# Optimization experiments

Hardware: AMD Instinct MI355X
Metric: run time of the kernel (lower is better)

Reference implementation:

```python
import jax, jax.numpy as jnp
import numpy as np

BLOCK = 128
SPARSE_BLOCK = 128
SF = 4
NEG = jnp.finfo(jnp.float32).min


def _unfold(x, size, step):
    # x: (..., T, d) -> (..., b, size, d) overlapping windows (torch unfold + transpose)
    b = (x.shape[-2] - size) // step + 1
    idx = np.arange(b)[:, None] * step + np.arange(size)
    return x[..., idx, :]


def _pad_tokens(x, s, pad_value):
    cfg = [(0, 0)] * (x.ndim - 2) + [(s, s), (0, 0)]
    return jnp.pad(x, cfg, constant_values=pad_value)


def _local_blocks(x, pad_value):
    size, step = BLOCK * 3, BLOCK
    s = (size - step) // 2
    return _unfold(_pad_tokens(x, s, pad_value), size, step)


def _sparse_blocks(x, pad_value):
    size0, step = SPARSE_BLOCK * 3, BLOCK // SF
    odd = step % 2
    size = size0 * 2
    s = (size - step) // 2 + odd
    xw = _unfold(_pad_tokens(x, s, pad_value), size, step)
    if odd:
        xw = xw[..., :-1, :, :]
    u = (size - BLOCK * 3 // SF) // 2 + odd
    sb = SPARSE_BLOCK
    u_ = u + odd
    return jnp.concatenate([xw[..., u - sb:u, :], xw[..., -u_:-u_ + sb, :]], axis=-2)


def _cat_gsl(x_global, x_sparse, x_local):
    # x_local: (n,h,b,t_loc,d); broadcast global over block axis
    b = x_local.shape[-3]
    g = jnp.broadcast_to(x_global[..., None, :, :],
                         x_global.shape[:-2] + (b,) + x_global.shape[-2:])
    return jnp.concatenate([g, x_sparse, x_local], axis=-2)


def _build_lsg(x, x_sparse, x_global, pad_value):
    loc = _local_blocks(x, pad_value)
    sp = _sparse_blocks(x_sparse, pad_value)
    return _cat_gsl(x_global, sp, loc)


def reference(query_layer, key_layer, value_layer, attention_mask,
              sparse_key, sparse_value, sparse_mask,
              global_key, global_value, global_mask):
    n, h, t, d = query_layer.shape
    n_blocks = t // BLOCK

    keys = _build_lsg(key_layer, sparse_key, global_key, 0.0)      # (n,h,b,K,d)
    vals = _build_lsg(value_layer, sparse_value, global_value, 0.0)

    # masks: (n,1,1,T) treated as d=1 token data after transpose
    m = jnp.swapaxes(attention_mask, -1, -2)    # (n,1,t,1)
    sm = jnp.swapaxes(sparse_mask, -1, -2)      # (n,1,t/SF,1)
    gm = jnp.swapaxes(global_mask, -1, -2)      # (n,1,g,1)
    mask = _build_lsg(m, sm, gm, NEG)           # (n,1,b,K,1)
    mask = jnp.swapaxes(mask, -1, -2)           # (n,1,b,1,K)

    q = query_layer.reshape(n, h, n_blocks, BLOCK, d)
    scores = jnp.einsum('nhbqd,nhbkd->nhbqk', q, keys) / jnp.sqrt(jnp.float32(d))
    probs = jax.nn.softmax(scores + mask, axis=-1)
    ctx = jnp.einsum('nhbqk,nhbkd->nhbqd', probs, vals)
    return ctx.reshape(n, h, t, d)


def setup_inputs() -> dict:
    key = jax.random.key(0)
    n, h, t, d = 2, 12, 4096, 64
    g = 64
    ts = t // SF
    k = jax.random.split(key, 7)
    return {
        'query_layer': jax.random.normal(k[0], (n, h, t, d), jnp.float32),
        'key_layer': jax.random.normal(k[1], (n, h, t, d), jnp.float32),
        'value_layer': jax.random.normal(k[2], (n, h, t, d), jnp.float32),
        'attention_mask': jnp.zeros((n, 1, 1, t), jnp.float32),
        'sparse_key': jax.random.normal(k[3], (n, h, ts, d), jnp.float32),
        'sparse_value': jax.random.normal(k[4], (n, h, ts, d), jnp.float32),
        'sparse_mask': jnp.zeros((n, 1, 1, ts), jnp.float32),
        'global_key': jax.random.normal(k[5], (n, h, g, d), jnp.float32),
        'global_value': jax.random.normal(k[6], (n, h, g, d), jnp.float32),
        'global_mask': jnp.zeros((n, 1, 1, g), jnp.float32),
    }
```

## Files before the change

kernel.cpp:

```cpp
#include <hip/hip_runtime.h>
#include <hip/hip_bf16.h>

typedef __attribute__((ext_vector_type(8))) short short8;
typedef __attribute__((ext_vector_type(4))) float f32x4;
typedef __attribute__((ext_vector_type(4))) unsigned u32x4;

#define LOG2E 1.44269504f
#define SCL2  0.18033688f
#define MNEG  -3.0e38f
#define MINIT -1.0e30f

__device__ __forceinline__ short f2bf(float f) {
  union { float f; unsigned u; } x; x.f = f;
  return (short)((x.u + 0x7FFFu + ((x.u >> 16) & 1u)) >> 16);
}
__device__ __forceinline__ float exp2g(float x) {
  float r; asm("v_exp_f32 %0, %1" : "=v"(r) : "v"(x)); return r;
}
__device__ __forceinline__ unsigned cvt_pk_bf16(float lo, float hi) {
  unsigned r;
  asm("v_cvt_pk_bf16_f32 %0, %1, %2" : "=v"(r) : "v"(lo), "v"(hi));
  return r;
}

__device__ __forceinline__ void conv_one(
    const float* __restrict__ src, short* __restrict__ dst,
    int Tin, int pad, int cid) {
  int Tpad = Tin + 2 * pad;
  int row = cid >> 3;
  int d0 = (cid & 7) * 8;
  int tok = row % Tpad;
  int nh = row / Tpad;
  int st = tok - pad;
  short8 o;
  if (st >= 0 && st < Tin) {
    const float4* sp = (const float4*)(src + ((size_t)nh * Tin + st) * 64 + d0);
    float4 f0 = sp[0], f1 = sp[1];
    o[0] = f2bf(f0.x); o[1] = f2bf(f0.y); o[2] = f2bf(f0.z); o[3] = f2bf(f0.w);
    o[4] = f2bf(f1.x); o[5] = f2bf(f1.y); o[6] = f2bf(f1.z); o[7] = f2bf(f1.w);
  } else {
#pragma unroll
    for (int j = 0; j < 8; ++j) o[j] = 0;
  }
  *(short8*)(dst + (size_t)row * 64 + d0) = o;
}

__device__ __forceinline__ void transv_one(
    const float* __restrict__ src, short* __restrict__ dst,
    int Tin, int pad, int tiles, int bidx, int tid, short (*lt)[72]) {
  int tile = bidx % tiles;
  int nh = bidx / tiles;
  int Tpad = Tin + 2 * pad;
  int c0 = tile * 64;
  int tok = tid >> 2;
  int dc = (tid & 3) * 16;
  int st = c0 + tok - pad;
  if (st >= 0 && st < Tin) {
    const float4* sp = (const float4*)(src + ((size_t)nh * Tin + st) * 64 + dc);
#pragma unroll
    for (int i = 0; i < 4; ++i) {
      float4 f = sp[i];
      lt[tok][dc + i * 4 + 0] = f2bf(f.x);
      lt[tok][dc + i * 4 + 1] = f2bf(f.y);
      lt[tok][dc + i * 4 + 2] = f2bf(f.z);
      lt[tok][dc + i * 4 + 3] = f2bf(f.w);
    }
  } else {
#pragma unroll
    for (int i = 0; i < 16; ++i) lt[tok][dc + i] = 0;
  }
  __syncthreads();
  int d = tid >> 2;
  int tc = (tid & 3) * 16;
  short8 o0, o1;
#pragma unroll
  for (int j = 0; j < 8; ++j) { o0[j] = lt[tc + j][d]; o1[j] = lt[tc + 8 + j][d]; }
  short* dp = dst + ((size_t)nh * 64 + d) * Tpad + c0 + tc;
  *(short8*)(dp) = o0;
  *(short8*)(dp + 8) = o1;
}

__global__ __launch_bounds__(256) void prepass_all(
    const float* __restrict__ K, const float* __restrict__ SK,
    const float* __restrict__ GK,
    const float* __restrict__ V, const float* __restrict__ SV,
    const float* __restrict__ GV,
    short* __restrict__ KL, short* __restrict__ KS, short* __restrict__ KG,
    short* __restrict__ VTL, short* __restrict__ VTS, short* __restrict__ VTG,
    const float* __restrict__ am, const float* __restrict__ sm,
    const float* __restrict__ gm,
    float* __restrict__ AM2, float* __restrict__ SM2, float* __restrict__ GM2) {
  __shared__ short lt[64][72];
  int bidx = blockIdx.x;
  int tid = threadIdx.x;
  if (bidx < 3264) { conv_one(K,  KL, 4096, 128, bidx * 256 + tid); return; }
  bidx -= 3264;
  if (bidx < 1008) { conv_one(SK, KS, 1024, 160, bidx * 256 + tid); return; }
  bidx -= 1008;
  if (bidx < 48)   { conv_one(GK, KG, 64, 0, bidx * 256 + tid); return; }
  bidx -= 48;
  if (bidx < 1632) { transv_one(V,  VTL, 4096, 128, 68, bidx, tid, lt); return; }
  bidx -= 1632;
  if (bidx < 504)  { transv_one(SV, VTS, 1024, 160, 21, bidx, tid, lt); return; }
  bidx -= 504;
  if (bidx < 24)   { transv_one(GV, VTG, 64, 0, 1, bidx, tid, lt); return; }
  bidx -= 24;
  int i = bidx * 256 + tid;
  if (i < 2 * 4352) {
    int n = i / 4352, rr = i % 4352, s = rr - 128;
    AM2[i] = (s >= 0 && s < 4096) ? am[n * 4096 + s] * LOG2E : MNEG;
  } else if (i < 2 * 4352 + 2 * 1344) {
    int j = i - 2 * 4352;
    int n = j / 1344, rr = j % 1344, s = rr - 160;
    SM2[j] = (s >= 0 && s < 1024) ? sm[n * 1024 + s] * LOG2E : MNEG;
  } else {
    int j = i - 2 * 4352 - 2 * 1344;
    GM2[j] = gm[j] * LOG2E;
  }
}

__global__ __launch_bounds__(512, 4) void lsg_attn9(
    const short* __restrict__ KL, const short* __restrict__ VTL,
    const short* __restrict__ KS, const short* __restrict__ VTS,
    const short* __restrict__ KG, const short* __restrict__ VTG,
    const float* __restrict__ AM2, const float* __restrict__ SM2,
    const float* __restrict__ GM2,
    const float* __restrict__ q_, float* __restrict__ out) {
  constexpr int TPL = 4352, TPS = 1344;
  __shared__ __align__(16) char smem[35328];

  int bid = blockIdx.x;
  bid = (bid & 7) * 96 + (bid >> 3);
  const int b = bid & 31, nh = bid >> 5, n_ = nh / 12;
  const int tid = threadIdx.x;
  const int wid = tid >> 6, lane = tid & 63;
  const int c = lane & 15, g = lane >> 4;
  const int r = tid >> 3, ch = tid & 7;
  const int skey = ((r >> 5) << 5) | (((r >> 2) & 3) << 3) |
                   (((r >> 4) & 1) << 2) | (r & 3);
  float* sclw = (float*)(smem + 32768) + wid * 16;
  const unsigned stg = ((unsigned)r << 7) + ((unsigned)(ch * 16) ^ ((unsigned)(r & 7) << 4));

  unsigned long long enc = 0; int nt = 0;
  {
    auto push = [&](int t) { enc |= (unsigned long long)t << (4 * nt); ++nt; };
    push(0);
    if (b >= 4)  push(1);
    if (b >= 2)  push(2);
    if (b <= 29) push(3);
    if (b <= 27) push(4);
    if (b >= 1)  { push(5); push(6); }
    push(7); push(8);
    if (b <= 30) { push(9); push(10); }
  }

  const float* qb = q_ + ((size_t)nh * 4096 + (size_t)b * 128 + wid * 16) * 64;
  short8 qa[2];
#pragma unroll
  for (int kc = 0; kc < 2; ++kc) {
    const float* qp = qb + (size_t)c * 64 + kc * 32 + g * 8;
    float4 f0 = *(const float4*)(qp);
    float4 f1 = *(const float4*)(qp + 4);
    short8 tq;
    tq[0] = f2bf(f0.x); tq[1] = f2bf(f0.y); tq[2] = f2bf(f0.z); tq[3] = f2bf(f0.w);
    tq[4] = f2bf(f1.x); tq[5] = f2bf(f1.y); tq[6] = f2bf(f1.z); tq[7] = f2bf(f1.w);
    qa[kc] = tq;
  }

  f32x4 acc[4];
#pragma unroll
  for (int dd = 0; dd < 4; ++dd) acc[dd] = f32x4{0.f, 0.f, 0.f, 0.f};
  float mrun = MINIT, lrun = 0.f;

  auto src_for = [&](int t, const short*& kp, const short*& vp,
                     const float*& mp, int& stride) {
    if (t == 0) {
      kp = KG + (size_t)nh * (64 * 64);
      vp = VTG + (size_t)nh * (64 * 64);
      mp = GM2 + n_ * 64;
      stride = 64;
    } else if (t <= 4) {
      int r0 = b * 32 + (t - 1) * 64 + (t >= 3 ? 96 : 0);
      kp = KS + ((size_t)nh * TPS + r0) * 64;
      vp = VTS + (size_t)nh * (64 * TPS) + r0;
      mp = SM2 + n_ * TPS + r0;
      stride = TPS;
    } else {
      int r0 = b * 128 + (t - 5) * 64;
      kp = KL + ((size_t)nh * TPL + r0) * 64;
      vp = VTL + (size_t)nh * (64 * TPL) + r0;
      mp = AM2 + n_ * TPL + r0;
      stride = TPL;
    }
  };

  short8 kr, vr;

  {
    const short* kp; const short* vp; const float* mp; int st;
    src_for(0, kp, vp, mp, st);
    kr = *(const short8*)(kp + skey * 64 + ch * 8);
    vr = *(const short8*)(vp + (size_t)r * st + ch * 8);
    *(short8*)(smem + stg) = kr;
    *(short8*)(smem + 16384 + stg) = vr;
    src_for((int)((enc >> 4) & 15ull), kp, vp, mp, st);
    kr = *(const short8*)(kp + skey * 64 + ch * 8);
    vr = *(const short8*)(vp + (size_t)r * st + ch * 8);
  }

  for (int i = 0; i < nt; ++i) {
    asm volatile("s_waitcnt lgkmcnt(0)\n\ts_barrier" ::: "memory");
    const int cur = i & 1, nxt = cur ^ 1;
    char* kbuf = smem + cur * 8192;
    char* vbuf = smem + 16384 + cur * 8192;

    f32x4 mk[4];
    {
      int tl = (int)((enc >> (4 * i)) & 15ull);
      const short* kp; const short* vp; const float* mp; int st;
      src_for(tl, kp, vp, mp, st);
#pragma unroll
      for (int kt = 0; kt < 4; ++kt)
        mk[kt] = *(const f32x4*)(mp + ((kt >> 1) << 5) + g * 8 + ((kt & 1) << 2));
    }

    short8 bk[4][2];
#pragma unroll
    for (int kt = 0; kt < 4; ++kt)
#pragma unroll
      for (int kc = 0; kc < 2; ++kc) {
        unsigned off = ((unsigned)(kt * 16 + c) << 7) +
                       ((unsigned)(kc * 64 + g * 16) ^ ((unsigned)(c & 7) << 4));
        bk[kt][kc] = *(const short8*)(kbuf + off);
      }

    if (i + 1 < nt) {
      *(short8*)(smem + nxt * 8192 + stg) = kr;
      *(short8*)(smem + 16384 + nxt * 8192 + stg) = vr;
    }
    if (i + 2 < nt) {
      int tn = (int)((enc >> (4 * (i + 2))) & 15ull);
      const short* kp; const short* vp; const float* mp; int st;
      src_for(tn, kp, vp, mp, st);
      kr = *(const short8*)(kp + skey * 64 + ch * 8);
      vr = *(const short8*)(vp + (size_t)r * st + ch * 8);
    }

    f32x4 s4[4];
    __builtin_amdgcn_s_setprio(1);
#pragma unroll
    for (int kt = 0; kt < 4; ++kt) {
      f32x4 z = f32x4{0.f, 0.f, 0.f, 0.f};
      z = __builtin_amdgcn_mfma_f32_16x16x32_bf16(bk[kt][0], qa[0], z, 0, 0, 0);
      z = __builtin_amdgcn_mfma_f32_16x16x32_bf16(bk[kt][1], qa[1], z, 0, 0, 0);
      s4[kt] = z;
    }
    __builtin_amdgcn_s_setprio(0);
#pragma unroll
    for (int kt = 0; kt < 4; ++kt)
#pragma unroll
      for (int j = 0; j < 4; ++j)
        s4[kt][j] = fmaf(s4[kt][j], SCL2, mk[kt][j]);

    float rs = 0.f;
    f32x4 p4[4];
#pragma unroll
    for (int kt = 0; kt < 4; ++kt)
#pragma unroll
      for (int j = 0; j < 4; ++j) {
        float p = exp2g(s4[kt][j] - mrun);
        p4[kt][j] = p;
        rs += p;
      }

    if (__any(rs > 4096.f)) {
      float tv = s4[0][0];
#pragma unroll
      for (int kt = 0; kt < 4; ++kt)
#pragma unroll
        for (int j = 0; j < 4; ++j) tv = fmaxf(tv, s4[kt][j]);
      tv = fmaxf(tv, __shfl_xor(tv, 16));
      tv = fmaxf(tv, __shfl_xor(tv, 32));
      float mn = fmaxf(mrun, tv);
      float sc = exp2g(mrun - mn);
      if (lane < 16) sclw[lane] = sc;
      rs = 0.f;
#pragma unroll
      for (int kt = 0; kt < 4; ++kt)
#pragma unroll
        for (int j = 0; j < 4; ++j) {
          float p = exp2g(s4[kt][j] - mn);
          p4[kt][j] = p;
          rs += p;
        }
      lrun = lrun * sc + rs;
      mrun = mn;
      f32x4 sq = *(const f32x4*)&sclw[4 * g];
#pragma unroll
      for (int dd = 0; dd < 4; ++dd)
#pragma unroll
        for (int j = 0; j < 4; ++j) acc[dd][j] *= sq[j];
    } else {
      lrun += rs;
    }

#pragma unroll
    for (int kk = 0; kk < 2; ++kk) {
      u32x4 uu;
      uu[0] = cvt_pk_bf16(p4[2 * kk][0], p4[2 * kk][1]);
      uu[1] = cvt_pk_bf16(p4[2 * kk][2], p4[2 * kk][3]);
      uu[2] = cvt_pk_bf16(p4[2 * kk + 1][0], p4[2 * kk + 1][1]);
      uu[3] = cvt_pk_bf16(p4[2 * kk + 1][2], p4[2 * kk + 1][3]);
      short8 pa = __builtin_bit_cast(short8, uu);
      __builtin_amdgcn_s_setprio(1);
#pragma unroll
      for (int dd = 0; dd < 4; ++dd) {
        unsigned voff = ((unsigned)(dd * 16 + c) << 7) +
                        ((unsigned)(kk * 64 + g * 16) ^ ((unsigned)(c & 7) << 4));
        short8 bv = *(const short8*)(vbuf + voff);
        acc[dd] = __builtin_amdgcn_mfma_f32_16x16x32_bf16(pa, bv, acc[dd], 0, 0, 0);
      }
      __builtin_amdgcn_s_setprio(0);
    }
  }

  float l = lrun;
  l += __shfl_xor(l, 16);
  l += __shfl_xor(l, 32);
  if (lane < 16) sclw[lane] = 1.f / l;
  f32x4 iv = *(const f32x4*)&sclw[4 * g];
  __syncthreads();
  float* fst = (float*)smem + wid * (16 * 68);
#pragma unroll
  for (int j = 0; j < 4; ++j)
#pragma unroll
    for (int dd = 0; dd < 4; ++dd)
      fst[(4 * g + j) * 68 + dd * 16 + c] = acc[dd][j] * iv[j];
  int rr = lane >> 2, cc = lane & 3;
  const float* fs = (float*)smem + wid * (16 * 68) + rr * 68 + cc * 16;
  float* op = out + ((size_t)nh * 4096 + (size_t)b * 128 + wid * 16 + rr) * 64 + cc * 16;
#pragma unroll
  for (int i = 0; i < 4; ++i)
    *(float4*)(op + i * 4) = *(const float4*)(fs + i * 4);
}

__global__ __launch_bounds__(256) void lsg_attn_fb(
    const float* __restrict__ q_,  const float* __restrict__ k_,
    const float* __restrict__ v_,  const float* __restrict__ amask,
    const float* __restrict__ sk,  const float* __restrict__ sv,
    const float* __restrict__ smk, const float* __restrict__ gk,
    const float* __restrict__ gv,  const float* __restrict__ gmk,
    float* __restrict__ out) {
  constexpr int T = 4096, D = 64, TS = 1024;
  constexpr float NEGF = -3.402823466e38f;
  __shared__ __align__(16) short k_lds[32][72];
  __shared__ __align__(16) short v_lds[64][40];
  __shared__ __align__(16) short p_lds[4][32][40];
  __shared__ float m_lds[32];
  const int bid = blockIdx.x;
  const int b = bid & 31, nh = bid >> 5, n_ = nh / 12;
  const int tid = threadIdx.x, wid = tid >> 6, lane = tid & 63;
  const int c = lane & 15, g = lane >> 4;
  const float* qb = q_ + ((size_t)nh * T + (size_t)b * 128) * D;
  const float* kb = k_ + (size_t)nh * T * D;
  const float* vb = v_ + (size_t)nh * T * D;
  const float* skb = sk + (size_t)nh * TS * D;
  const float* svb = sv + (size_t)nh * TS * D;
  const float* gkb = gk + (size_t)nh * 64 * D;
  const float* gvb = gv + (size_t)nh * 64 * D;
  const float* am = amask + (size_t)n_ * T;
  const float* sm = smk + (size_t)n_ * TS;
  const float* gm = gmk + (size_t)n_ * 64;
  short8 qa[2][2];
#pragma unroll
  for (int mt = 0; mt < 2; ++mt)
#pragma unroll
    for (int kc = 0; kc < 2; ++kc) {
      const float* qp = qb + (size_t)(wid * 32 + mt * 16 + c) * D + kc * 32 + g * 8;
      short8 t;
#pragma unroll
      for (int j = 0; j < 8; ++j) t[j] = f2bf(qp[j]);
      qa[mt][kc] = t;
    }
  f32x4 acc[2][4];
#pragma unroll
  for (int mt = 0; mt < 2; ++mt)
#pragma unroll
    for (int dd = 0; dd < 4; ++dd) acc[mt][dd] = f32x4{0.f, 0.f, 0.f, 0.f};
  float mrun[2][4], lrun[2][4];
#pragma unroll
  for (int mt = 0; mt < 2; ++mt)
#pragma unroll
    for (int j = 0; j < 4; ++j) { mrun[mt][j] = NEGF; lrun[mt][j] = 0.f; }
  const int key_local = tid >> 3;
  const int seg = tid & 7;
  const int d0 = seg * 8;
  for (int tile = 0; tile < 22; ++tile) {
    __syncthreads();
    {
      const int kk = tile * 32 + key_local;
      const float* ksrc; const float* vsrc; float mval; bool valid;
      if (kk < 64) {
        ksrc = gkb + kk * D; vsrc = gvb + kk * D; mval = gm[kk]; valid = true;
      } else if (kk < 320) {
        int s = b * 32 - 160 + (kk - 64) + ((kk >= 192) ? 96 : 0);
        valid = (s >= 0) && (s < TS);
        int sc2 = valid ? s : 0;
        ksrc = skb + sc2 * D; vsrc = svb + sc2 * D;
        mval = valid ? sm[sc2] : NEGF;
      } else {
        int tt = b * 128 - 128 + (kk - 320);
        valid = (tt >= 0) && (tt < T);
        int tc = valid ? tt : 0;
        ksrc = kb + tc * D; vsrc = vb + tc * D;
        mval = valid ? am[tc] : NEGF;
      }
      short8 k8; short v8[8];
      if (valid) {
#pragma unroll
        for (int j = 0; j < 8; ++j) { k8[j] = f2bf(ksrc[d0 + j]); v8[j] = f2bf(vsrc[d0 + j]); }
      } else {
#pragma unroll
        for (int j = 0; j < 8; ++j) { k8[j] = 0; v8[j] = 0; }
      }
      *(short8*)(&k_lds[key_local][d0]) = k8;
#pragma unroll
      for (int j = 0; j < 8; ++j) v_lds[d0 + j][key_local] = v8[j];
      if (seg == 0) m_lds[key_local] = mval;
    }
    __syncthreads();
    short8 bk[2][2];
#pragma unroll
    for (int kt = 0; kt < 2; ++kt)
#pragma unroll
      for (int kc = 0; kc < 2; ++kc)
        bk[kt][kc] = *(const short8*)(&k_lds[kt * 16 + c][kc * 32 + g * 8]);
    f32x4 s_[2][2];
#pragma unroll
    for (int mt = 0; mt < 2; ++mt)
#pragma unroll
      for (int kt = 0; kt < 2; ++kt) {
        f32x4 z = f32x4{0.f, 0.f, 0.f, 0.f};
        z = __builtin_amdgcn_mfma_f32_16x16x32_bf16(qa[mt][0], bk[kt][0], z, 0, 0, 0);
        z = __builtin_amdgcn_mfma_f32_16x16x32_bf16(qa[mt][1], bk[kt][1], z, 0, 0, 0);
        s_[mt][kt] = z;
      }
    const float msk0 = m_lds[c];
    const float msk1 = m_lds[16 + c];
#pragma unroll
    for (int mt = 0; mt < 2; ++mt) {
#pragma unroll
      for (int j = 0; j < 4; ++j) {
        float s0 = s_[mt][0][j] * 0.125f + msk0;
        float s1 = s_[mt][1][j] * 0.125f + msk1;
        float tv = fmaxf(s0, s1);
        tv = fmaxf(tv, __shfl_xor(tv, 1));
        tv = fmaxf(tv, __shfl_xor(tv, 2));
        tv = fmaxf(tv, __shfl_xor(tv, 4));
        tv = fmaxf(tv, __shfl_xor(tv, 8));
        float mold = mrun[mt][j];
        float mnew = fmaxf(mold, tv);
        float scale = __expf(mold - mnew);
        mrun[mt][j] = mnew;
        float p0 = __expf(s0 - mnew);
        float p1 = __expf(s1 - mnew);
        lrun[mt][j] = lrun[mt][j] * scale + p0 + p1;
#pragma unroll
        for (int dd = 0; dd < 4; ++dd) acc[mt][dd][j] *= scale;
        p_lds[wid][mt * 16 + g * 4 + j][c] = f2bf(p0);
        p_lds[wid][mt * 16 + g * 4 + j][16 + c] = f2bf(p1);
      }
    }
    __syncthreads();
#pragma unroll
    for (int mt = 0; mt < 2; ++mt) {
      short8 pa = *(const short8*)(&p_lds[wid][mt * 16 + c][g * 8]);
#pragma unroll
      for (int dd = 0; dd < 4; ++dd) {
        short8 bv = *(const short8*)(&v_lds[dd * 16 + c][g * 8]);
        acc[mt][dd] = __builtin_amdgcn_mfma_f32_16x16x32_bf16(pa, bv, acc[mt][dd], 0, 0, 0);
      }
    }
  }
  float* ob = out + ((size_t)nh * T + (size_t)b * 128 + (size_t)wid * 32) * D;
#pragma unroll
  for (int mt = 0; mt < 2; ++mt)
#pragma unroll
    for (int j = 0; j < 4; ++j) {
      float l = lrun[mt][j];
      l += __shfl_xor(l, 1);
      l += __shfl_xor(l, 2);
      l += __shfl_xor(l, 4);
      l += __shfl_xor(l, 8);
      float inv = 1.f / l;
      int row = mt * 16 + g * 4 + j;
#pragma unroll
      for (int dd = 0; dd < 4; ++dd)
        ob[(size_t)row * D + dd * 16 + c] = acc[mt][dd][j] * inv;
    }
}

extern "C" void kernel_launch(void* const* d_in, const int* in_sizes, int n_in,
                              void* d_out, int out_size, void* d_ws, size_t ws_size,
                              hipStream_t stream) {
  const float* q  = (const float*)d_in[0];
  const float* k  = (const float*)d_in[1];
  const float* v  = (const float*)d_in[2];
  const float* am = (const float*)d_in[3];
  const float* sk = (const float*)d_in[4];
  const float* sv = (const float*)d_in[5];
  const float* sm = (const float*)d_in[6];
  const float* gk = (const float*)d_in[7];
  const float* gv = (const float*)d_in[8];
  const float* gm = (const float*)d_in[9];
  float* out = (float*)d_out;

  size_t off = 0;
  char* base = (char*)d_ws;
  auto alloc = [&](size_t bytes) { void* p = base + off; off += bytes; return p; };
  short* KL  = (short*)alloc(13369344);
  short* VTL = (short*)alloc(13369344);
  short* KS  = (short*)alloc(4128768);
  short* VTS = (short*)alloc(4128768);
  short* KG  = (short*)alloc(196608);
  short* VTG = (short*)alloc(196608);
  float* AM2 = (float*)alloc(34816);
  float* SM2 = (float*)alloc(10752);
  float* GM2 = (float*)alloc(512);

  if (off <= ws_size) {
    hipLaunchKernelGGL(prepass_all, dim3(6525), dim3(256), 0, stream,
                       k, sk, gk, v, sv, gv, KL, KS, KG, VTL, VTS, VTG,
                       am, sm, gm, AM2, SM2, GM2);
    hipLaunchKernelGGL(lsg_attn9, dim3(768), dim3(512), 0, stream,
                       KL, VTL, KS, VTS, KG, VTG, AM2, SM2, GM2, q, out);
  } else {
    hipLaunchKernelGGL(lsg_attn_fb, dim3(768), dim3(256), 0, stream,
                       q, k, v, am, sk, sv, sm, gk, gv, gm, out);
  }
}
```

Baseline: 58.74 us.

## Give each wave two query tiles to reuse K/V fragments, fold scale into K

The attention kernel now runs 4 waves of 256 threads, each owning 32 query rows (two 16-row MFMA tiles), so each K and V fragment read from LDS feeds two MFMAs. The softmax scale is applied to keys during the bf16 conversion prepass, and the mask is used as the MFMA accumulator init, which drops the per-score fma. The aim is fewer LDS reads per MFMA and less VALU work. In exchange each wave holds more registers (two accumulator sets), the launch bounds drop to 3 blocks per CU, and there are fewer waves to hide latency.

```diff
diff --git a/kernel.cpp b/kernel.cpp
--- a/kernel.cpp
+++ b/kernel.cpp
@@ -36,8 +36,10 @@
   if (st >= 0 && st < Tin) {
     const float4* sp = (const float4*)(src + ((size_t)nh * Tin + st) * 64 + d0);
     float4 f0 = sp[0], f1 = sp[1];
-    o[0] = f2bf(f0.x); o[1] = f2bf(f0.y); o[2] = f2bf(f0.z); o[3] = f2bf(f0.w);
-    o[4] = f2bf(f1.x); o[5] = f2bf(f1.y); o[6] = f2bf(f1.z); o[7] = f2bf(f1.w);
+    o[0] = f2bf(f0.x * SCL2); o[1] = f2bf(f0.y * SCL2);
+    o[2] = f2bf(f0.z * SCL2); o[3] = f2bf(f0.w * SCL2);
+    o[4] = f2bf(f1.x * SCL2); o[5] = f2bf(f1.y * SCL2);
+    o[6] = f2bf(f1.z * SCL2); o[7] = f2bf(f1.w * SCL2);
   } else {
 #pragma unroll
     for (int j = 0; j < 8; ++j) o[j] = 0;
@@ -119,7 +121,7 @@
   }
 }
 
-__global__ __launch_bounds__(512, 4) void lsg_attn9(
+__global__ __launch_bounds__(256, 3) void lsg_attn10(
     const short* __restrict__ KL, const short* __restrict__ VTL,
     const short* __restrict__ KS, const short* __restrict__ VTS,
     const short* __restrict__ KG, const short* __restrict__ VTG,
@@ -135,11 +137,12 @@
   const int tid = threadIdx.x;
   const int wid = tid >> 6, lane = tid & 63;
   const int c = lane & 15, g = lane >> 4;
-  const int r = tid >> 3, ch = tid & 7;
+  const int r = tid >> 2, ch = tid & 3;
   const int skey = ((r >> 5) << 5) | (((r >> 2) & 3) << 3) |
                    (((r >> 4) & 1) << 2) | (r & 3);
-  float* sclw = (float*)(smem + 32768) + wid * 16;
-  const unsigned stg = ((unsigned)r << 7) + ((unsigned)(ch * 16) ^ ((unsigned)(r & 7) << 4));
+  float* sclw = (float*)(smem + 32768) + wid * 32;
+  const unsigned stg0 = ((unsigned)r << 7) + ((unsigned)(ch * 16) ^ ((unsigned)(r & 7) << 4));
+  const unsigned stg1 = ((unsigned)r << 7) + ((unsigned)((ch + 4) * 16) ^ ((unsigned)(r & 7) << 4));
 
   unsigned long long enc = 0; int nt = 0;
   {
@@ -154,23 +157,27 @@
     if (b <= 30) { push(9); push(10); }
   }
 
-  const float* qb = q_ + ((size_t)nh * 4096 + (size_t)b * 128 + wid * 16) * 64;
-  short8 qa[2];
-#pragma unroll
-  for (int kc = 0; kc < 2; ++kc) {
-    const float* qp = qb + (size_t)c * 64 + kc * 32 + g * 8;
-    float4 f0 = *(const float4*)(qp);
-    float4 f1 = *(const float4*)(qp + 4);
-    short8 tq;
-    tq[0] = f2bf(f0.x); tq[1] = f2bf(f0.y); tq[2] = f2bf(f0.z); tq[3] = f2bf(f0.w);
-    tq[4] = f2bf(f1.x); tq[5] = f2bf(f1.y); tq[6] = f2bf(f1.z); tq[7] = f2bf(f1.w);
-    qa[kc] = tq;
-  }
-
-  f32x4 acc[4];
-#pragma unroll
-  for (int dd = 0; dd < 4; ++dd) acc[dd] = f32x4{0.f, 0.f, 0.f, 0.f};
-  float mrun = MINIT, lrun = 0.f;
+  const float* qb = q_ + ((size_t)nh * 4096 + (size_t)b * 128 + wid * 32) * 64;
+  short8 qa[2][2];
+#pragma unroll
+  for (int mt = 0; mt < 2; ++mt)
+#pragma unroll
+    for (int kc = 0; kc < 2; ++kc) {
+      const float* qp = qb + (size_t)(mt * 16 + c) * 64 + kc * 32 + g * 8;
+      float4 f0 = *(const float4*)(qp);
+      float4 f1 = *(const float4*)(qp + 4);
+      short8 tq;
+      tq[0] = f2bf(f0.x); tq[1] = f2bf(f0.y); tq[2] = f2bf(f0.z); tq[3] = f2bf(f0.w);
+      tq[4] = f2bf(f1.x); tq[5] = f2bf(f1.y); tq[6] = f2bf(f1.z); tq[7] = f2bf(f1.w);
+      qa[mt][kc] = tq;
+    }
+
+  f32x4 acc[2][4];
+#pragma unroll
+  for (int mt = 0; mt < 2; ++mt)
+#pragma unroll
+    for (int dd = 0; dd < 4; ++dd) acc[mt][dd] = f32x4{0.f, 0.f, 0.f, 0.f};
+  float mrun[2] = {MINIT, MINIT}, lrun[2] = {0.f, 0.f};
 
   auto src_for = [&](int t, const short*& kp, const short*& vp,
                      const float*& mp, int& stride) {
@@ -194,18 +201,24 @@
     }
   };
 
-  short8 kr, vr;
+  short8 kr0, kr1, vr0, vr1;
 
   {
     const short* kp; const short* vp; const float* mp; int st;
     src_for(0, kp, vp, mp, st);
-    kr = *(const short8*)(kp + skey * 64 + ch * 8);
-    vr = *(const short8*)(vp + (size_t)r * st + ch * 8);
-    *(short8*)(smem + stg) = kr;
-    *(short8*)(smem + 16384 + stg) = vr;
+    kr0 = *(const short8*)(kp + skey * 64 + ch * 8);
+    kr1 = *(const short8*)(kp + skey * 64 + (ch + 4) * 8);
+    vr0 = *(const short8*)(vp + (size_t)r * st + ch * 8);
+    vr1 = *(const short8*)(vp + (size_t)r * st + (ch + 4) * 8);
+    *(short8*)(smem + stg0) = kr0;
+    *(short8*)(smem + stg1) = kr1;
+    *(short8*)(smem + 16384 + stg0) = vr0;
+    *(short8*)(smem + 16384 + stg1) = vr1;
     src_for((int)((enc >> 4) & 15ull), kp, vp, mp, st);
-    kr = *(const short8*)(kp + skey * 64 + ch * 8);
-    vr = *(const short8*)(vp + (size_t)r * st + ch * 8);
+    kr0 = *(const short8*)(kp + skey * 64 + ch * 8);
+    kr1 = *(const short8*)(kp + skey * 64 + (ch + 4) * 8);
+    vr0 = *(const short8*)(vp + (size_t)r * st + ch * 8);
+    vr1 = *(const short8*)(vp + (size_t)r * st + (ch + 4) * 8);
   }
 
   for (int i = 0; i < nt; ++i) {
@@ -224,123 +237,139 @@
         mk[kt] = *(const f32x4*)(mp + ((kt >> 1) << 5) + g * 8 + ((kt & 1) << 2));
     }
 
-    short8 bk[4][2];
-#pragma unroll
-    for (int kt = 0; kt < 4; ++kt)
-#pragma unroll
-      for (int kc = 0; kc < 2; ++kc) {
-        unsigned off = ((unsigned)(kt * 16 + c) << 7) +
-                       ((unsigned)(kc * 64 + g * 16) ^ ((unsigned)(c & 7) << 4));
-        bk[kt][kc] = *(const short8*)(kbuf + off);
-      }
+    f32x4 s40[4], s41[4];
+    __builtin_amdgcn_s_setprio(1);
+#pragma unroll
+    for (int kt = 0; kt < 4; ++kt) {
+      unsigned off0 = ((unsigned)(kt * 16 + c) << 7) +
+                      ((unsigned)(g * 16) ^ ((unsigned)(c & 7) << 4));
+      unsigned off1 = ((unsigned)(kt * 16 + c) << 7) +
+                      ((unsigned)(64 + g * 16) ^ ((unsigned)(c & 7) << 4));
+      short8 bk0 = *(const short8*)(kbuf + off0);
+      short8 bk1 = *(const short8*)(kbuf + off1);
+      f32x4 z0 = __builtin_amdgcn_mfma_f32_16x16x32_bf16(bk0, qa[0][0], mk[kt], 0, 0, 0);
+      z0 = __builtin_amdgcn_mfma_f32_16x16x32_bf16(bk1, qa[0][1], z0, 0, 0, 0);
+      s40[kt] = z0;
+      f32x4 z1 = __builtin_amdgcn_mfma_f32_16x16x32_bf16(bk0, qa[1][0], mk[kt], 0, 0, 0);
+      z1 = __builtin_amdgcn_mfma_f32_16x16x32_bf16(bk1, qa[1][1], z1, 0, 0, 0);
+      s41[kt] = z1;
+    }
+    __builtin_amdgcn_s_setprio(0);
 
     if (i + 1 < nt) {
-      *(short8*)(smem + nxt * 8192 + stg) = kr;
-      *(short8*)(smem + 16384 + nxt * 8192 + stg) = vr;
+      *(short8*)(smem + nxt * 8192 + stg0) = kr0;
+      *(short8*)(smem + nxt * 8192 + stg1) = kr1;
+      *(short8*)(smem + 16384 + nxt * 8192 + stg0) = vr0;
+      *(short8*)(smem + 16384 + nxt * 8192 + stg1) = vr1;
     }
     if (i + 2 < nt) {
       int tn = (int)((enc >> (4 * (i + 2))) & 15ull);
       const short* kp; const short* vp; const float* mp; int st;
       src_for(tn, kp, vp, mp, st);
-      kr = *(const short8*)(kp + skey * 64 + ch * 8);
-      vr = *(const short8*)(vp + (size_t)r * st + ch * 8);
-    }
-
-    f32x4 s4[4];
-    __builtin_amdgcn_s_setprio(1);
-#pragma unroll
-    for (int kt = 0; kt < 4; ++kt) {
-      f32x4 z = f32x4{0.f, 0.f, 0.f, 0.f};
-      z = __builtin_amdgcn_mfma_f32_16x16x32_bf16(bk[kt][0], qa[0], z, 0, 0, 0);
-      z = __builtin_amdgcn_mfma_f32_16x16x32_bf16(bk[kt][1], qa[1], z, 0, 0, 0);
-      s4[kt] = z;
-    }
-    __builtin_amdgcn_s_setprio(0);
+      kr0 = *(const short8*)(kp + skey * 64 + ch * 8);
+      kr1 = *(const short8*)(kp + skey * 64 + (ch + 4) * 8);
+      vr0 = *(const short8*)(vp + (size_t)r * st + ch * 8);
+      vr1 = *(const short8*)(vp + (size_t)r * st + (ch + 4) * 8);
+    }
+
+    f32x4 p40[4], p41[4];
+    float rs0 = 0.f, rs1 = 0.f;
 #pragma unroll
     for (int kt = 0; kt < 4; ++kt)
 #pragma unroll
-      for (int j = 0; j < 4; ++j)
-        s4[kt][j] = fmaf(s4[kt][j], SCL2, mk[kt][j]);
-
-    float rs = 0.f;
-    f32x4 p4[4];
-#pragma unroll
-    for (int kt = 0; kt < 4; ++kt)
-#pragma unroll
       for (int j = 0; j < 4; ++j) {
-        float p = exp2g(s4[kt][j] - mrun);
-        p4[kt][j] = p;
-        rs += p;
-      }
-
-    if (__any(rs > 4096.f)) {
-      float tv = s4[0][0];
-#pragma unroll
-      for (int kt = 0; kt < 4; ++kt)
-#pragma unroll
-        for (int j = 0; j < 4; ++j) tv = fmaxf(tv, s4[kt][j]);
-      tv = fmaxf(tv, __shfl_xor(tv, 16));
-      tv = fmaxf(tv, __shfl_xor(tv, 32));
-      float mn = fmaxf(mrun, tv);
-      float sc = exp2g(mrun - mn);
-      if (lane < 16) sclw[lane] = sc;
-      rs = 0.f;
-#pragma unroll
-      for (int kt = 0; kt < 4; ++kt)
-#pragma unroll
-        for (int j = 0; j < 4; ++j) {
-          float p = exp2g(s4[kt][j] - mn);
-          p4[kt][j] = p;
-          rs += p;
-        }
-      lrun = lrun * sc + rs;
-      mrun = mn;
-      f32x4 sq = *(const f32x4*)&sclw[4 * g];
-#pragma unroll
-      for (int dd = 0; dd < 4; ++dd)
-#pragma unroll
-        for (int j = 0; j < 4; ++j) acc[dd][j] *= sq[j];
+        float p0 = exp2g(s40[kt][j] - mrun[0]);
+        float p1 = exp2g(s41[kt][j] - mrun[1]);
+        p40[kt][j] = p0; rs0 += p0;
+        p41[kt][j] = p1; rs1 += p1;
+      }
+
+    if (__any(fmaxf(rs0, rs1) > 4096.f)) {
+#pragma unroll
+      for (int mt = 0; mt < 2; ++mt) {
+        f32x4* s4 = mt ? s41 : s40;
+        f32x4* p4 = mt ? p41 : p40;
+        float tv = s4[0][0];
+#pragma unroll
+        for (int kt = 0; kt < 4; ++kt)
+#pragma unroll
+          for (int j = 0; j < 4; ++j) tv = fmaxf(tv, s4[kt][j]);
+        tv = fmaxf(tv, __shfl_xor(tv, 16));
+        tv = fmaxf(tv, __shfl_xor(tv, 32));
+        float mn = fmaxf(mrun[mt], tv);
+        float sc = exp2g(mrun[mt] - mn);
+        if (lane < 16) sclw[mt * 16 + lane] = sc;
+        float rs = 0.f;
+#pragma unroll
+        for (int kt = 0; kt < 4; ++kt)
+#pragma unroll
+          for (int j = 0; j < 4; ++j) {
+            float p = exp2g(s4[kt][j] - mn);
+            p4[kt][j] = p;
+            rs += p;
+          }
+        lrun[mt] = lrun[mt] * sc + rs;
+        mrun[mt] = mn;
+        f32x4 sq = *(const f32x4*)&sclw[mt * 16 + 4 * g];
+#pragma unroll
+        for (int dd = 0; dd < 4; ++dd)
+#pragma unroll
+          for (int j = 0; j < 4; ++j) acc[mt][dd][j] *= sq[j];
+      }
     } else {
-      lrun += rs;
+      lrun[0] += rs0;
+      lrun[1] += rs1;
     }
 
 #pragma unroll
     for (int kk = 0; kk < 2; ++kk) {
-      u32x4 uu;
-      uu[0] = cvt_pk_bf16(p4[2 * kk][0], p4[2 * kk][1]);
-      uu[1] = cvt_pk_bf16(p4[2 * kk][2], p4[2 * kk][3]);
-      uu[2] = cvt_pk_bf16(p4[2 * kk + 1][0], p4[2 * kk + 1][1]);
-      uu[3] = cvt_pk_bf16(p4[2 * kk + 1][2], p4[2 * kk + 1][3]);
-      short8 pa = __builtin_bit_cast(short8, uu);
+      u32x4 u0, u1;
+      u0[0] = cvt_pk_bf16(p40[2 * kk][0], p40[2 * kk][1]);
+      u0[1] = cvt_pk_bf16(p40[2 * kk][2], p40[2 * kk][3]);
+      u0[2] = cvt_pk_bf16(p40[2 * kk + 1][0], p40[2 * kk + 1][1]);
+      u0[3] = cvt_pk_bf16(p40[2 * kk + 1][2], p40[2 * kk + 1][3]);
+      u1[0] = cvt_pk_bf16(p41[2 * kk][0], p41[2 * kk][1]);
+      u1[1] = cvt_pk_bf16(p41[2 * kk][2], p41[2 * kk][3]);
+      u1[2] = cvt_pk_bf16(p41[2 * kk + 1][0], p41[2 * kk + 1][1]);
+      u1[3] = cvt_pk_bf16(p41[2 * kk + 1][2], p41[2 * kk + 1][3]);
+      short8 pa0 = __builtin_bit_cast(short8, u0);
+      short8 pa1 = __builtin_bit_cast(short8, u1);
       __builtin_amdgcn_s_setprio(1);
 #pragma unroll
       for (int dd = 0; dd < 4; ++dd) {
         unsigned voff = ((unsigned)(dd * 16 + c) << 7) +
                         ((unsigned)(kk * 64 + g * 16) ^ ((unsigned)(c & 7) << 4));
         short8 bv = *(const short8*)(vbuf + voff);
-        acc[dd] = __builtin_amdgcn_mfma_f32_16x16x32_bf16(pa, bv, acc[dd], 0, 0, 0);
+        acc[0][dd] = __builtin_amdgcn_mfma_f32_16x16x32_bf16(pa0, bv, acc[0][dd], 0, 0, 0);
+        acc[1][dd] = __builtin_amdgcn_mfma_f32_16x16x32_bf16(pa1, bv, acc[1][dd], 0, 0, 0);
       }
       __builtin_amdgcn_s_setprio(0);
     }
   }
 
-  float l = lrun;
-  l += __shfl_xor(l, 16);
-  l += __shfl_xor(l, 32);
-  if (lane < 16) sclw[lane] = 1.f / l;
-  f32x4 iv = *(const f32x4*)&sclw[4 * g];
+  f32x4 iv[2];
+#pragma unroll
+  for (int mt = 0; mt < 2; ++mt) {
+    float l = lrun[mt];
+    l += __shfl_xor(l, 16);
+    l += __shfl_xor(l, 32);
+    if (lane < 16) sclw[mt * 16 + lane] = 1.f / l;
+    iv[mt] = *(const f32x4*)&sclw[mt * 16 + 4 * g];
+  }
   __syncthreads();
-  float* fst = (float*)smem + wid * (16 * 68);
-#pragma unroll
-  for (int j = 0; j < 4; ++j)
-#pragma unroll
-    for (int dd = 0; dd < 4; ++dd)
-      fst[(4 * g + j) * 68 + dd * 16 + c] = acc[dd][j] * iv[j];
-  int rr = lane >> 2, cc = lane & 3;
-  const float* fs = (float*)smem + wid * (16 * 68) + rr * 68 + cc * 16;
-  float* op = out + ((size_t)nh * 4096 + (size_t)b * 128 + wid * 16 + rr) * 64 + cc * 16;
-#pragma unroll
-  for (int i = 0; i < 4; ++i)
+  float* fst = (float*)smem + wid * (32 * 68);
+#pragma unroll
+  for (int mt = 0; mt < 2; ++mt)
+#pragma unroll
+    for (int j = 0; j < 4; ++j)
+#pragma unroll
+      for (int dd = 0; dd < 4; ++dd)
+        fst[(mt * 16 + 4 * g + j) * 68 + dd * 16 + c] = acc[mt][dd][j] * iv[mt][j];
+  int rr = lane >> 1, hh = lane & 1;
+  const float* fs = fst + rr * 68 + hh * 32;
+  float* op = out + ((size_t)nh * 4096 + (size_t)b * 128 + wid * 32 + rr) * 64 + hh * 32;
+#pragma unroll
+  for (int i = 0; i < 8; ++i)
     *(float4*)(op + i * 4) = *(const float4*)(fs + i * 4);
 }
 
@@ -532,7 +561,7 @@
     hipLaunchKernelGGL(prepass_all, dim3(6525), dim3(256), 0, stream,
                        k, sk, gk, v, sv, gv, KL, KS, KG, VTL, VTS, VTG,
                        am, sm, gm, AM2, SM2, GM2);
-    hipLaunchKernelGGL(lsg_attn9, dim3(768), dim3(512), 0, stream,
+    hipLaunchKernelGGL(lsg_attn10, dim3(768), dim3(256), 0, stream,
                        KL, VTL, KS, VTS, KG, VTG, AM2, SM2, GM2, q, out);
   } else {
     hipLaunchKernelGGL(lsg_attn_fb, dim3(768), dim3(256), 0, stream,
```

New measurement: 83.14 us. 41.5% more time.
